# Kernel optimization log

Hardware: AMD Instinct MI355X
Metric: run time of the kernel (lower is better)

## Reference

```python
import jax, jax.numpy as jnp
import numpy as np

N = 100000
E = 1600000
H = 128
M = 256
L = 6
G = 512          # number of graphs in the batch
A = 95           # num_atom_types
EXTRA = 3        # input_dim - 1
EPS = 1e-5


def swish(x):
    return x * jax.nn.sigmoid(x)


def setup_inputs() -> dict:
    key = jax.random.key(0)
    ks = jax.random.split(key, 16)
    z = jax.random.randint(ks[0], (N, 1), 0, A).astype(jnp.float32)
    extra = jax.random.normal(ks[1], (N, EXTRA), dtype=jnp.float32)
    x = jnp.concatenate([z, extra], axis=1)                     # [N, 4]
    edge_index = jax.random.randint(ks[2], (2, E), 0, N)        # [2, E]
    batch = jnp.sort(jax.random.randint(ks[3], (N,), 0, G))     # [N]
    s = 0.02
    z_embed = jax.random.normal(ks[4], (A, H), dtype=jnp.float32) * s
    extra_w = jax.random.normal(ks[5], (H, EXTRA), dtype=jnp.float32) * (1.0 / np.sqrt(EXTRA))
    extra_b = jnp.zeros((H,), jnp.float32)
    conv_w = jax.random.normal(ks[6], (L, H, H), dtype=jnp.float32) * (1.0 / np.sqrt(H))
    conv_b = jnp.zeros((L, H), jnp.float32)
    gamma = jnp.ones((L, H), jnp.float32)
    beta = jnp.zeros((L, H), jnp.float32)
    mean_scale = jnp.ones((L, H), jnp.float32)
    mlp_w1 = jax.random.normal(ks[7], (L, M, H), dtype=jnp.float32) * (1.0 / np.sqrt(H))
    mlp_b1 = jnp.zeros((L, M), jnp.float32)
    mlp_w2 = jax.random.normal(ks[8], (L, H, M), dtype=jnp.float32) * (1.0 / np.sqrt(M))
    mlp_b2 = jnp.zeros((L, H), jnp.float32)
    return dict(x=x, edge_index=edge_index, batch=batch, z_embed=z_embed,
                extra_w=extra_w, extra_b=extra_b, conv_w=conv_w, conv_b=conv_b,
                gamma=gamma, beta=beta, mean_scale=mean_scale,
                mlp_w1=mlp_w1, mlp_b1=mlp_b1, mlp_w2=mlp_w2, mlp_b2=mlp_b2)


def gnn_forward(x, edge_index, batch, z_embed, extra_w, extra_b, conv_w, conv_b,
                gamma, beta, mean_scale, mlp_w1, mlp_b1, mlp_w2, mlp_b2):
    z = x[:, 0].astype(jnp.int32)
    h = z_embed[z] + x[:, 1:] @ extra_w.T + extra_b                 # [N, H]

    # GCN: add self loops, symmetric normalization (computed once; graph is static)
    loop = jnp.arange(N)
    src = jnp.concatenate([edge_index[0], loop])
    dst = jnp.concatenate([edge_index[1], loop])
    deg = jax.ops.segment_sum(jnp.ones_like(dst, jnp.float32), dst, num_segments=N)
    dinv = jnp.where(deg > 0, jax.lax.rsqrt(jnp.maximum(deg, 1.0)), 0.0)
    norm = (dinv[src] * dinv[dst])[:, None]                         # [E+N, 1]

    cnt = jax.ops.segment_sum(jnp.ones((N,), jnp.float32), batch, num_segments=G)[:, None]
    cnt = jnp.maximum(cnt, 1.0)

    for i in range(L):
        h_res = h
        # GCNConv
        xw = h @ conv_w[i].T
        agg = jax.ops.segment_sum(xw[src] * norm, dst, num_segments=N) + conv_b[i]
        # GraphNorm: gamma * (x - alpha*mean) / sqrt(var + eps) + beta, per graph
        mean = jax.ops.segment_sum(agg, batch, num_segments=G) / cnt   # [G, H]
        sub = agg - mean_scale[i] * mean[batch]
        var = jax.ops.segment_sum(sub * sub, batch, num_segments=G) / cnt
        hn = gamma[i] * sub * jax.lax.rsqrt(var[batch] + EPS) + beta[i]
        ha = swish(hn)
        # residual MLP
        h = swish(swish(ha @ mlp_w1[i].T + mlp_b1[i]) @ mlp_w2[i].T + mlp_b2[i]) + h_res
    return h


def reference(x, edge_index, batch, z_embed, extra_w, extra_b, conv_w, conv_b,
              gamma, beta, mean_scale, mlp_w1, mlp_b1, mlp_w2, mlp_b2):
    return gnn_forward(x, edge_index, batch, z_embed, extra_w, extra_b, conv_w, conv_b,
                       gamma, beta, mean_scale, mlp_w1, mlp_b1, mlp_w2, mlp_b2)
```

## Files before the change

kernel.cpp:

```cpp
#include <hip/hip_runtime.h>

#define NN 100000
#define EE 1600000
#define HH 128
#define MM 256
#define LL 6
#define GG 512
#define SCAN_NB ((NN + 1023) / 1024)

typedef __attribute__((ext_vector_type(8))) short short8;
typedef __attribute__((ext_vector_type(4))) float floatx4;

__device__ __forceinline__ float swishf(float v) {
    return v / (1.0f + __expf(-v));
}

__device__ __forceinline__ unsigned short f2bf(float f) {
    unsigned u = __builtin_bit_cast(unsigned, f);
    unsigned r = u + 0x7FFFu + ((u >> 16) & 1u);
    return (unsigned short)(r >> 16);
}

__device__ __forceinline__ float bf2f(unsigned short u) {
    return __builtin_bit_cast(float, (unsigned)u << 16);
}

__device__ __forceinline__ float2 bf2f2(unsigned u) {
    float2 r;
    r.x = __builtin_bit_cast(float, u << 16);
    r.y = __builtin_bit_cast(float, u & 0xFFFF0000u);
    return r;
}

__device__ __forceinline__ void unpack8(uint4 v, float* a) {
    float2 p0 = bf2f2(v.x), p1 = bf2f2(v.y), p2 = bf2f2(v.z), p3 = bf2f2(v.w);
    a[0] = p0.x; a[1] = p0.y; a[2] = p1.x; a[3] = p1.y;
    a[4] = p2.x; a[5] = p2.y; a[6] = p3.x; a[7] = p3.y;
}

__device__ __forceinline__ uint4 pack8(const float* o) {
    uint4 pk;
    pk.x = (unsigned)f2bf(o[0]) | ((unsigned)f2bf(o[1]) << 16);
    pk.y = (unsigned)f2bf(o[2]) | ((unsigned)f2bf(o[3]) << 16);
    pk.z = (unsigned)f2bf(o[4]) | ((unsigned)f2bf(o[5]) << 16);
    pk.w = (unsigned)f2bf(o[6]) | ((unsigned)f2bf(o[7]) << 16);
    return pk;
}

__device__ __forceinline__ uint2 pack4(const float* o) {
    uint2 pk;
    pk.x = (unsigned)f2bf(o[0]) | ((unsigned)f2bf(o[1]) << 16);
    pk.y = (unsigned)f2bf(o[2]) | ((unsigned)f2bf(o[3]) << 16);
    return pk;
}

__global__ void k_embed(const float* __restrict__ x, const float* __restrict__ z_embed,
                        const float* __restrict__ ew, const float* __restrict__ eb,
                        unsigned short* __restrict__ hb) {
    int idx = blockIdx.x * blockDim.x + threadIdx.x;
    if (idx >= NN * 32) return;
    int n = idx >> 5;
    int c0 = (idx & 31) << 2;
    const float* xr = x + (size_t)n * 4;
    int z = (int)xr[0];
    float x1 = xr[1], x2 = xr[2], x3 = xr[3];
    const float* ze = z_embed + (size_t)z * HH + c0;
    float o[4];
#pragma unroll
    for (int j = 0; j < 4; ++j) {
        int c = c0 + j;
        o[j] = ze[j] + x1 * ew[c * 3 + 0] + x2 * ew[c * 3 + 1] + x3 * ew[c * 3 + 2] + eb[c];
    }
    *(uint2*)(hb + (size_t)n * HH + c0) = pack4(o);
}

__global__ void k_f2bf3(const float* __restrict__ s1, unsigned short* __restrict__ d1, int n1,
                        const float* __restrict__ s2, unsigned short* __restrict__ d2, int n2,
                        const float* __restrict__ s3, unsigned short* __restrict__ d3, int n3) {
    int i = blockIdx.x * blockDim.x + threadIdx.x;
    if (i < n1) {
        d1[i] = f2bf(s1[i]);
    } else if (i < n1 + n2) {
        d2[i - n1] = f2bf(s2[i - n1]);
    } else if (i < n1 + n2 + n3) {
        d3[i - n1 - n2] = f2bf(s3[i - n1 - n2]);
    }
}

__global__ __launch_bounds__(256) void k_degree_p(const int* __restrict__ dst,
                                                  int* __restrict__ deg) {
    int part = blockIdx.x & 7;
    int blk = blockIdx.x >> 3;
    int nb = gridDim.x >> 3;
    int lo = (int)((long long)part * NN / 8);
    int hi = (int)((long long)(part + 1) * NN / 8);
    for (int e = blk * 256 + threadIdx.x; e < EE; e += nb * 256) {
        int d = dst[e];
        if (d >= lo && d < hi) atomicAdd(&deg[d], 1);
    }
}

__global__ void k_dinv(const int* __restrict__ deg, float* __restrict__ dinv) {
    int n = blockIdx.x * blockDim.x + threadIdx.x;
    if (n < NN) dinv[n] = rsqrtf((float)(deg[n] + 1));
}

__global__ void k_scan1(const int* __restrict__ deg, int* __restrict__ bsum) {
    __shared__ int sd[256];
    int t = threadIdx.x;
    int base = blockIdx.x * 1024 + t * 4;
    int s = 0;
#pragma unroll
    for (int j = 0; j < 4; ++j) {
        int i = base + j;
        if (i < NN) s += deg[i];
    }
    sd[t] = s;
    __syncthreads();
    for (int off = 128; off > 0; off >>= 1) {
        if (t < off) sd[t] += sd[t + off];
        __syncthreads();
    }
    if (t == 0) bsum[blockIdx.x] = sd[0];
}

__global__ void k_scan2(const int* __restrict__ bsum, int* __restrict__ boff) {
    __shared__ int sd[128];
    int t = threadIdx.x;
    int v = (t < SCAN_NB) ? bsum[t] : 0;
    sd[t] = v;
    __syncthreads();
    for (int off = 1; off < 128; off <<= 1) {
        int u = (t >= off) ? sd[t - off] : 0;
        __syncthreads();
        sd[t] += u;
        __syncthreads();
    }
    boff[t] = sd[t] - v;
}

__global__ void k_scan3(const int* __restrict__ deg, const int* __restrict__ boff,
                        int* __restrict__ rowptr) {
    __shared__ int sd[256];
    int t = threadIdx.x;
    int base = blockIdx.x * 1024 + t * 4;
    int v[4];
    int s = 0;
#pragma unroll
    for (int j = 0; j < 4; ++j) {
        int i = base + j;
        v[j] = (i < NN) ? deg[i] : 0;
        s += v[j];
    }
    sd[t] = s;
    __syncthreads();
    for (int off = 1; off < 256; off <<= 1) {
        int u = (t >= off) ? sd[t - off] : 0;
        __syncthreads();
        sd[t] += u;
        __syncthreads();
    }
    int run = boff[blockIdx.x] + sd[t] - s;
#pragma unroll
    for (int j = 0; j < 4; ++j) {
        int i = base + j;
        if (i < NN) rowptr[i] = run;
        if (i == NN - 1) rowptr[NN] = run + v[j];
        run += v[j];
    }
}

__global__ __launch_bounds__(256) void k_fill_p(const int* __restrict__ ei,
                                                const int* __restrict__ rowptr,
                                                int* __restrict__ cursor,
                                                int* __restrict__ col) {
    int part = blockIdx.x & 7;
    int blk = blockIdx.x >> 3;
    int nb = gridDim.x >> 3;
    int lo = (int)((long long)part * NN / 8);
    int hi = (int)((long long)(part + 1) * NN / 8);
    for (int e = blk * 256 + threadIdx.x; e < EE; e += nb * 256) {
        int d = ei[EE + e];
        if (d >= lo && d < hi) {
            int p = atomicAdd(&cursor[d], 1);
            col[rowptr[d] + p] = ei[e];
        }
    }
}

__global__ void k_gptr(const int* __restrict__ batch, int* __restrict__ gptr) {
    int n = blockIdx.x * blockDim.x + threadIdx.x;
    if (n >= NN) return;
    int b = batch[n];
    int pb = (n == 0) ? -1 : batch[n - 1];
    for (int g = pb + 1; g <= b; ++g) gptr[g] = n;
    if (n == NN - 1) {
        for (int g = b + 1; g <= GG; ++g) gptr[g] = NN;
    }
}

__global__ __launch_bounds__(256) void k_conv(const unsigned short* __restrict__ A,
                                              const unsigned short* __restrict__ B,
                                              const float* __restrict__ dinv,
                                              unsigned short* __restrict__ Cb) {
    __shared__ unsigned short Bs[128][HH + 8];
    const int tid = threadIdx.x;
    const int wave = tid >> 6;
    const int lane = tid & 63;
    const int quad = lane >> 4;
    const int l16 = lane & 15;
    const int wr = (wave & 1) << 6;
    const int wc = (wave >> 1) << 6;
    const int rowBase = blockIdx.x * 128;

    for (int i = tid; i < 128 * (HH / 8); i += 256) {
        int r = i / (HH / 8);
        int kk = (i % (HH / 8)) * 8;
        int rho = (r & 64) | ((r & 3) << 4) | ((r >> 2) & 15);
        *(uint4*)(&Bs[rho][kk]) = *(const uint4*)(B + (size_t)r * HH + kk);
    }

    floatx4 acc[4][4];
    const floatx4 zed = {0.f, 0.f, 0.f, 0.f};
#pragma unroll
    for (int i = 0; i < 4; ++i)
#pragma unroll
        for (int j = 0; j < 4; ++j) acc[i][j] = zed;

    int ar[4];
#pragma unroll
    for (int i = 0; i < 4; ++i) {
        int r = rowBase + wr + (i << 4) + l16;
        ar[i] = r < NN ? r : NN - 1;
    }

    __syncthreads();

#pragma unroll
    for (int ks = 0; ks < HH / 32; ++ks) {
        int k = (ks << 5) + (quad << 3);
        short8 a[4], b[4];
#pragma unroll
        for (int i = 0; i < 4; ++i) a[i] = *(const short8*)(A + (size_t)ar[i] * HH + k);
#pragma unroll
        for (int j = 0; j < 4; ++j) b[j] = *(const short8*)(&Bs[wc + (j << 4) + l16][k]);
#pragma unroll
        for (int i = 0; i < 4; ++i)
#pragma unroll
            for (int j = 0; j < 4; ++j)
                acc[i][j] =
                    __builtin_amdgcn_mfma_f32_16x16x32_bf16(a[i], b[j], acc[i][j], 0, 0, 0);
    }

    const int c0 = wc + (l16 << 2);
#pragma unroll
    for (int i = 0; i < 4; ++i) {
        int rb = rowBase + wr + (i << 4) + (quad << 2);
#pragma unroll
        for (int reg = 0; reg < 4; ++reg) {
            int r = rb + reg;
            if (r < NN) {
                float dv = dinv[r];
                float o[4];
#pragma unroll
                for (int j = 0; j < 4; ++j) o[j] = acc[i][j][reg] * dv;
                *(uint2*)(Cb + (size_t)r * HH + c0) = pack4(o);
            }
        }
    }
}

__global__ __launch_bounds__(256) void k_agg(const unsigned short* __restrict__ y,
                                             const int* __restrict__ rowptr,
                                             const int* __restrict__ col,
                                             const float* __restrict__ dinv,
                                             const float* __restrict__ cb,
                                             unsigned short* __restrict__ agg) {
    int w = threadIdx.x >> 6;
    int lane = threadIdx.x & 63;
    int d = blockIdx.x * 4 + w;
    if (d >= NN) return;
    int grp = lane >> 4;
    int l16 = lane & 15;
    const uint4* yv = (const uint4*)y;
    float acc[8];
#pragma unroll
    for (int j = 0; j < 8; ++j) acc[j] = 0.f;
    if (grp == 0) {
        uint4 v = yv[(size_t)d * 16 + l16];
        unpack8(v, acc);
    }
    int beg = rowptr[d];
    int end = rowptr[d + 1];
    for (int e = beg + grp; e < end; e += 4) {
        int s = col[e];
        uint4 v = yv[(size_t)s * 16 + l16];
        float b0[8];
        unpack8(v, b0);
#pragma unroll
        for (int k = 0; k < 8; ++k) acc[k] += b0[k];
    }
#pragma unroll
    for (int j = 0; j < 8; ++j) {
        acc[j] += __shfl_xor(acc[j], 16, 64);
        acc[j] += __shfl_xor(acc[j], 32, 64);
    }
    if (grp == 0) {
        float dv = dinv[d];
        float4 c0 = *(const float4*)(cb + l16 * 8);
        float4 c1 = *(const float4*)(cb + l16 * 8 + 4);
        float o[8];
        o[0] = acc[0] * dv + c0.x; o[1] = acc[1] * dv + c0.y;
        o[2] = acc[2] * dv + c0.z; o[3] = acc[3] * dv + c0.w;
        o[4] = acc[4] * dv + c1.x; o[5] = acc[5] * dv + c1.y;
        o[6] = acc[6] * dv + c1.z; o[7] = acc[7] * dv + c1.w;
        *(uint4*)(agg + (size_t)d * HH + l16 * 8) = pack8(o);
    }
}

__global__ __launch_bounds__(512) void k_stats(const unsigned short* __restrict__ agg,
                                               const int* __restrict__ gptr,
                                               const float* __restrict__ ms,
                                               const float* __restrict__ gamma,
                                               const float* __restrict__ beta,
                                               float* __restrict__ c1,
                                               float* __restrict__ c0) {
    __shared__ float s1[512];
    __shared__ float s2[512];
    int g = blockIdx.x;
    int t = threadIdx.x;
    int c = t & 127;
    int part = t >> 7;
    int beg = gptr[g];
    int end = gptr[g + 1];
    float S1 = 0.f, S2 = 0.f;
    for (int n = beg + part; n < end; n += 4) {
        float v = bf2f(agg[(size_t)n * HH + c]);
        S1 += v;
        S2 += v * v;
    }
    s1[t] = S1;
    s2[t] = S2;
    __syncthreads();
    if (part == 0) {
        S1 = (s1[c] + s1[c + 128]) + (s1[c + 256] + s1[c + 384]);
        S2 = (s2[c] + s2[c + 128]) + (s2[c + 256] + s2[c + 384]);
        int cnt = end - beg;
        float inv = 1.0f / (float)(cnt > 0 ? cnt : 1);
        float m = S1 * inv;
        float msc = ms[c];
        float var = S2 * inv - msc * (2.0f - msc) * m * m;
        float rstd = rsqrtf(var + 1e-5f);
        float c1v = gamma[c] * rstd;
        c1[g * HH + c] = c1v;
        c0[g * HH + c] = beta[c] - c1v * msc * m;
    }
}

__global__ __launch_bounds__(256) void k_mega(const unsigned short* __restrict__ agg,
                                              const int* __restrict__ batch,
                                              const float* __restrict__ c1,
                                              const float* __restrict__ c0,
                                              const unsigned short* __restrict__ W1,
                                              const float* __restrict__ b1,
                                              const unsigned short* __restrict__ W2,
                                              const float* __restrict__ b2,
                                              const unsigned short* __restrict__ Wc,
                                              const float* __restrict__ dinv,
                                              unsigned short* __restrict__ hb,
                                              float* __restrict__ h_out,
                                              unsigned short* __restrict__ y_out, int writeF,
                                              int doConv) {
    __shared__ unsigned short smem[64 * (MM + 8)];
    const int tid = threadIdx.x;
    const int wave = tid >> 6;
    const int lane = tid & 63;
    const int quad = lane >> 4;
    const int l16 = lane & 15;
    const int wrh = (wave & 1) << 5;
    const int wch = (wave >> 1) << 7;
    const int wc2 = (wave >> 1) << 6;
    const int rowBase = blockIdx.x * 64;
    const floatx4 zed = {0.f, 0.f, 0.f, 0.f};

    int ar[2], gi[2];
#pragma unroll
    for (int i = 0; i < 2; ++i) {
        int r = rowBase + wrh + (i << 4) + l16;
        ar[i] = r < NN ? r : NN - 1;
        gi[i] = batch[ar[i]];
    }

    short8 a_all[4][2];
#pragma unroll
    for (int ks = 0; ks < 4; ++ks) {
        int k = (ks << 5) + (quad << 3);
#pragma unroll
        for (int i = 0; i < 2; ++i) {
            uint4 raw = *(const uint4*)(agg + (size_t)ar[i] * HH + k);
            float v[8];
            unpack8(raw, v);
            const float* c1p = c1 + gi[i] * HH + k;
            const float* c0p = c0 + gi[i] * HH + k;
            float4 c1a = *(const float4*)c1p;
            float4 c1b = *(const float4*)(c1p + 4);
            float4 c0a = *(const float4*)c0p;
            float4 c0b = *(const float4*)(c0p + 4);
            float cc1[8] = {c1a.x, c1a.y, c1a.z, c1a.w, c1b.x, c1b.y, c1b.z, c1b.w};
            float cc0[8] = {c0a.x, c0a.y, c0a.z, c0a.w, c0b.x, c0b.y, c0b.z, c0b.w};
            short8 av;
#pragma unroll
            for (int j = 0; j < 8; ++j)
                av[j] = (short)f2bf(swishf(cc1[j] * v[j] + cc0[j]));
            a_all[ks][i] = av;
        }
    }

    const int c0a = wch + (l16 << 3);
#pragma unroll
    for (int jh = 0; jh < 2; ++jh) {
        floatx4 acc1[2][4];
#pragma unroll
        for (int i = 0; i < 2; ++i)
#pragma unroll
            for (int j = 0; j < 4; ++j) acc1[i][j] = zed;
#pragma unroll
        for (int ks = 0; ks < 4; ++ks) {
            int k = (ks << 5) + (quad << 3);
            short8 b[4];
#pragma unroll
            for (int j = 0; j < 4; ++j) {
                int pc = c0a + (jh << 2) + j;
                b[j] = *(const short8*)(W1 + (size_t)pc * HH + k);
            }
#pragma unroll
            for (int i = 0; i < 2; ++i)
#pragma unroll
                for (int j = 0; j < 4; ++j)
                    acc1[i][j] = __builtin_amdgcn_mfma_f32_16x16x32_bf16(a_all[ks][i], b[j],
                                                                         acc1[i][j], 0, 0, 0);
        }
        float4 b4 = *(const float4*)(b1 + c0a + (jh << 2));
        float bv[4] = {b4.x, b4.y, b4.z, b4.w};
#pragma unroll
        for (int i = 0; i < 2; ++i) {
#pragma unroll
            for (int reg = 0; reg < 4; ++reg) {
                int lr = wrh + (i << 4) + (quad << 2) + reg;
                float o[4];
#pragma unroll
                for (int j = 0; j < 4; ++j) o[j] = swishf(acc1[i][j][reg] + bv[j]);
                *(uint2*)(&smem[lr * (MM + 8) + c0a + (jh << 2)]) = pack4(o);
            }
        }
    }
    __syncthreads();

    floatx4 acc2[2][4];
#pragma unroll
    for (int i = 0; i < 2; ++i)
#pragma unroll
        for (int j = 0; j < 4; ++j) acc2[i][j] = zed;
#pragma unroll
    for (int ks = 0; ks < MM / 32; ++ks) {
        int k = (ks << 5) + (quad << 3);
        short8 a[2], b[4];
#pragma unroll
        for (int i = 0; i < 2; ++i)
            a[i] = *(const short8*)(&smem[(wrh + (i << 4) + l16) * (MM + 8) + k]);
#pragma unroll
        for (int j = 0; j < 4; ++j) {
            int pc = wc2 + (l16 << 2) + j;
            b[j] = *(const short8*)(W2 + (size_t)pc * MM + k);
        }
#pragma unroll
        for (int i = 0; i < 2; ++i)
#pragma unroll
            for (int j = 0; j < 4; ++j)
                acc2[i][j] =
                    __builtin_amdgcn_mfma_f32_16x16x32_bf16(a[i], b[j], acc2[i][j], 0, 0, 0);
    }
    __syncthreads();

    const int co = wc2 + (l16 << 2);
    {
        float4 b4 = *(const float4*)(b2 + co);
        float bv[4] = {b4.x, b4.y, b4.z, b4.w};
#pragma unroll
        for (int i = 0; i < 2; ++i) {
            int rb = rowBase + wrh + (i << 4) + (quad << 2);
#pragma unroll
            for (int reg = 0; reg < 4; ++reg) {
                int r = rb + reg;
                if (r < NN) {
                    uint2 rv = *(const uint2*)(hb + (size_t)r * HH + co);
                    float2 r01 = bf2f2(rv.x), r23 = bf2f2(rv.y);
                    float o[4];
                    o[0] = swishf(acc2[i][0][reg] + bv[0]) + r01.x;
                    o[1] = swishf(acc2[i][1][reg] + bv[1]) + r01.y;
                    o[2] = swishf(acc2[i][2][reg] + bv[2]) + r23.x;
                    o[3] = swishf(acc2[i][3][reg] + bv[3]) + r23.y;
                    uint2 pk = pack4(o);
                    *(uint2*)(hb + (size_t)r * HH + co) = pk;
                    if (writeF)
                        *(float4*)(h_out + (size_t)r * HH + co) =
                            make_float4(o[0], o[1], o[2], o[3]);
                    int lr = wrh + (i << 4) + (quad << 2) + reg;
                    *(uint2*)(&smem[lr * 136 + co]) = pk;
                }
            }
        }
    }

    if (doConv) {
        __syncthreads();
        floatx4 acc3[2][4];
#pragma unroll
        for (int i = 0; i < 2; ++i)
#pragma unroll
            for (int j = 0; j < 4; ++j) acc3[i][j] = zed;
#pragma unroll
        for (int ks = 0; ks < 4; ++ks) {
            int k = (ks << 5) + (quad << 3);
            short8 a[2], b[4];
#pragma unroll
            for (int i = 0; i < 2; ++i)
                a[i] = *(const short8*)(&smem[(wrh + (i << 4) + l16) * 136 + k]);
#pragma unroll
            for (int j = 0; j < 4; ++j) {
                int pc = wc2 + (l16 << 2) + j;
                b[j] = *(const short8*)(Wc + (size_t)pc * HH + k);
            }
#pragma unroll
            for (int i = 0; i < 2; ++i)
#pragma unroll
                for (int j = 0; j < 4; ++j)
                    acc3[i][j] =
                        __builtin_amdgcn_mfma_f32_16x16x32_bf16(a[i], b[j], acc3[i][j], 0, 0, 0);
        }
#pragma unroll
        for (int i = 0; i < 2; ++i) {
            int rb = rowBase + wrh + (i << 4) + (quad << 2);
#pragma unroll
            for (int reg = 0; reg < 4; ++reg) {
                int r = rb + reg;
                if (r < NN) {
                    float dv = dinv[r];
                    float o[4];
#pragma unroll
                    for (int j = 0; j < 4; ++j) o[j] = acc3[i][j][reg] * dv;
                    *(uint2*)(y_out + (size_t)r * HH + co) = pack4(o);
                }
            }
        }
    }
}

extern "C" void kernel_launch(void* const* d_in, const int* in_sizes, int n_in,
                              void* d_out, int out_size, void* d_ws, size_t ws_size,
                              hipStream_t stream) {
    const float* x = (const float*)d_in[0];
    const int* ei = (const int*)d_in[1];
    const int* batch = (const int*)d_in[2];
    const float* z_embed = (const float*)d_in[3];
    const float* extra_w = (const float*)d_in[4];
    const float* extra_b = (const float*)d_in[5];
    const float* conv_w = (const float*)d_in[6];
    const float* conv_b = (const float*)d_in[7];
    const float* gamma = (const float*)d_in[8];
    const float* beta = (const float*)d_in[9];
    const float* mean_scale = (const float*)d_in[10];
    const float* mlp_w1 = (const float*)d_in[11];
    const float* mlp_b1 = (const float*)d_in[12];
    const float* mlp_w2 = (const float*)d_in[13];
    const float* mlp_b2 = (const float*)d_in[14];
    float* h_out = (float*)d_out;

    char* wsB = (char*)d_ws;
    size_t off = 0;
    auto alloc = [&](size_t bytes) -> void* {
        void* p = (void*)(wsB + off);
        off = (off + bytes + 255) & ~(size_t)255;
        return p;
    };
    float* dinv = (float*)alloc((size_t)NN * 4);
    int* deg = (int*)alloc((size_t)NN * 4);
    int* cursor = (int*)alloc((size_t)NN * 4);
    int* rowptr = (int*)alloc((size_t)(NN + 1) * 4);
    int* bsum = (int*)alloc(128 * 4);
    int* boff = (int*)alloc(128 * 4);
    int* col = (int*)alloc((size_t)EE * 4);
    int* gptr = (int*)alloc((size_t)(GG + 1) * 4);
    float* c1t = (float*)alloc((size_t)GG * HH * 4);
    float* c0t = (float*)alloc((size_t)GG * HH * 4);
    unsigned short* wb =
        (unsigned short*)alloc((size_t)(LL * (HH * HH + MM * HH + HH * MM)) * 2);
    unsigned short* cwb = wb;
    unsigned short* w1b = wb + (size_t)LL * HH * HH;
    unsigned short* w2b = w1b + (size_t)LL * MM * HH;
    unsigned short* hb = (unsigned short*)alloc((size_t)NN * HH * 2);
    unsigned short* ybuf = (unsigned short*)alloc((size_t)NN * HH * 2);
    unsigned short* aggb = (unsigned short*)alloc((size_t)NN * HH * 2);

    hipMemsetAsync(deg, 0, (size_t)NN * 4, stream);
    hipMemsetAsync(cursor, 0, (size_t)NN * 4, stream);

    k_embed<<<(NN * 32 + 255) / 256, 256, 0, stream>>>(x, z_embed, extra_w, extra_b, hb);
    {
        int n1 = LL * HH * HH, n2 = LL * MM * HH, n3 = LL * HH * MM;
        int nt = n1 + n2 + n3;
        k_f2bf3<<<(nt + 255) / 256, 256, 0, stream>>>(conv_w, cwb, n1, mlp_w1, w1b, n2,
                                                      mlp_w2, w2b, n3);
    }
    k_degree_p<<<1024, 256, 0, stream>>>(ei + EE, deg);
    k_dinv<<<(NN + 255) / 256, 256, 0, stream>>>(deg, dinv);
    k_scan1<<<SCAN_NB, 256, 0, stream>>>(deg, bsum);
    k_scan2<<<1, 128, 0, stream>>>(bsum, boff);
    k_scan3<<<SCAN_NB, 256, 0, stream>>>(deg, boff, rowptr);
    k_fill_p<<<1024, 256, 0, stream>>>(ei, rowptr, cursor, col);
    k_gptr<<<(NN + 255) / 256, 256, 0, stream>>>(batch, gptr);

    int gconv = (NN + 127) / 128;
    int gmega = (NN + 63) / 64;
    k_conv<<<gconv, 256, 0, stream>>>(hb, cwb, dinv, ybuf);
    for (int i = 0; i < LL; ++i) {
        k_agg<<<(NN + 3) / 4, 256, 0, stream>>>(ybuf, rowptr, col, dinv,
                                                conv_b + (size_t)i * HH, aggb);
        k_stats<<<GG, 512, 0, stream>>>(aggb, gptr, mean_scale + (size_t)i * HH,
                                        gamma + (size_t)i * HH, beta + (size_t)i * HH, c1t,
                                        c0t);
        k_mega<<<gmega, 256, 0, stream>>>(
            aggb, batch, c1t, c0t, w1b + (size_t)i * MM * HH, mlp_b1 + (size_t)i * MM,
            w2b + (size_t)i * HH * MM, mlp_b2 + (size_t)i * HH,
            cwb + (size_t)(i + 1 < LL ? i + 1 : 0) * HH * HH, dinv, hb, h_out, ybuf,
            i == LL - 1 ? 1 : 0, i < LL - 1 ? 1 : 0);
    }
}
```

Baseline: 1.416 ms.

## Stage normalized activations in LDS and retile first MLP GEMM per wave

The GraphNorm+swish prologue is now computed cooperatively (one row-quarter per thread) with coalesced loads and written to a dedicated LDS tile. The first MLP GEMM is retiled so each wave covers all 64 rows by 64 output columns, reading A from LDS. This cuts redundant W1 global loads and the duplicated c1/c0 fetches across waves. The cost is a separate LDS buffer, which raises LDS use and may lower occupancy, plus an extra barrier.

```diff
diff --git a/kernel.cpp b/kernel.cpp
--- a/kernel.cpp
+++ b/kernel.cpp
@@ -371,127 +371,118 @@
                                               float* __restrict__ h_out,
                                               unsigned short* __restrict__ y_out, int writeF,
                                               int doConv) {
-    __shared__ unsigned short smem[64 * (MM + 8)];
+    __shared__ unsigned short ha_s[64 * 136];
+    __shared__ unsigned short ts[64 * 264];
     const int tid = threadIdx.x;
     const int wave = tid >> 6;
     const int lane = tid & 63;
     const int quad = lane >> 4;
     const int l16 = lane & 15;
-    const int wrh = (wave & 1) << 5;
-    const int wch = (wave >> 1) << 7;
-    const int wc2 = (wave >> 1) << 6;
     const int rowBase = blockIdx.x * 64;
     const floatx4 zed = {0.f, 0.f, 0.f, 0.f};
 
-    int ar[2], gi[2];
-#pragma unroll
-    for (int i = 0; i < 2; ++i) {
-        int r = rowBase + wrh + (i << 4) + l16;
-        ar[i] = r < NN ? r : NN - 1;
-        gi[i] = batch[ar[i]];
-    }
-
-    short8 a_all[4][2];
-#pragma unroll
-    for (int ks = 0; ks < 4; ++ks) {
-        int k = (ks << 5) + (quad << 3);
-#pragma unroll
-        for (int i = 0; i < 2; ++i) {
-            uint4 raw = *(const uint4*)(agg + (size_t)ar[i] * HH + k);
+    {
+        int lr = tid >> 2;
+        int coff = (tid & 3) << 5;
+        int r = rowBase + lr;
+        if (r >= NN) r = NN - 1;
+        int g = batch[r];
+        const float* c1p = c1 + g * HH + coff;
+        const float* c0p = c0 + g * HH + coff;
+#pragma unroll
+        for (int q = 0; q < 4; ++q) {
+            uint4 raw = *(const uint4*)(agg + (size_t)r * HH + coff + (q << 3));
             float v[8];
             unpack8(raw, v);
-            const float* c1p = c1 + gi[i] * HH + k;
-            const float* c0p = c0 + gi[i] * HH + k;
-            float4 c1a = *(const float4*)c1p;
-            float4 c1b = *(const float4*)(c1p + 4);
-            float4 c0a = *(const float4*)c0p;
-            float4 c0b = *(const float4*)(c0p + 4);
-            float cc1[8] = {c1a.x, c1a.y, c1a.z, c1a.w, c1b.x, c1b.y, c1b.z, c1b.w};
-            float cc0[8] = {c0a.x, c0a.y, c0a.z, c0a.w, c0b.x, c0b.y, c0b.z, c0b.w};
-            short8 av;
-#pragma unroll
-            for (int j = 0; j < 8; ++j)
-                av[j] = (short)f2bf(swishf(cc1[j] * v[j] + cc0[j]));
-            a_all[ks][i] = av;
-        }
-    }
-
-    const int c0a = wch + (l16 << 3);
-#pragma unroll
-    for (int jh = 0; jh < 2; ++jh) {
-        floatx4 acc1[2][4];
-#pragma unroll
-        for (int i = 0; i < 2; ++i)
+            float4 ca = *(const float4*)(c1p + (q << 3));
+            float4 cb4 = *(const float4*)(c1p + (q << 3) + 4);
+            float4 da = *(const float4*)(c0p + (q << 3));
+            float4 db = *(const float4*)(c0p + (q << 3) + 4);
+            float cc1[8] = {ca.x, ca.y, ca.z, ca.w, cb4.x, cb4.y, cb4.z, cb4.w};
+            float cc0[8] = {da.x, da.y, da.z, da.w, db.x, db.y, db.z, db.w};
+            float o[8];
+#pragma unroll
+            for (int j = 0; j < 8; ++j) o[j] = swishf(cc1[j] * v[j] + cc0[j]);
+            *(uint4*)(&ha_s[lr * 136 + coff + (q << 3)]) = pack8(o);
+        }
+    }
+    __syncthreads();
+
+    {
+        const int wca = wave << 6;
+        floatx4 acc1[4][4];
+#pragma unroll
+        for (int i = 0; i < 4; ++i)
 #pragma unroll
             for (int j = 0; j < 4; ++j) acc1[i][j] = zed;
 #pragma unroll
         for (int ks = 0; ks < 4; ++ks) {
             int k = (ks << 5) + (quad << 3);
-            short8 b[4];
-#pragma unroll
-            for (int j = 0; j < 4; ++j) {
-                int pc = c0a + (jh << 2) + j;
-                b[j] = *(const short8*)(W1 + (size_t)pc * HH + k);
+            short8 a[4], b[4];
+#pragma unroll
+            for (int i = 0; i < 4; ++i)
+                a[i] = *(const short8*)(&ha_s[((i << 4) + l16) * 136 + k]);
+#pragma unroll
+            for (int j = 0; j < 4; ++j)
+                b[j] = *(const short8*)(W1 + (size_t)(wca + (l16 << 2) + j) * HH + k);
+#pragma unroll
+            for (int i = 0; i < 4; ++i)
+#pragma unroll
+                for (int j = 0; j < 4; ++j)
+                    acc1[i][j] =
+                        __builtin_amdgcn_mfma_f32_16x16x32_bf16(a[i], b[j], acc1[i][j], 0, 0, 0);
+        }
+        const int ct = wca + (l16 << 2);
+        float4 b4 = *(const float4*)(b1 + ct);
+        float bv[4] = {b4.x, b4.y, b4.z, b4.w};
+#pragma unroll
+        for (int i = 0; i < 4; ++i) {
+#pragma unroll
+            for (int reg = 0; reg < 4; ++reg) {
+                int lr = (i << 4) + (quad << 2) + reg;
+                float o[4];
+#pragma unroll
+                for (int j = 0; j < 4; ++j) o[j] = swishf(acc1[i][j][reg] + bv[j]);
+                *(uint2*)(&ts[lr * 264 + ct]) = pack4(o);
             }
+        }
+    }
+    __syncthreads();
+
+    const int wrb = (wave & 1) << 5;
+    const int wcb = (wave >> 1) << 6;
+    const int co = wcb + (l16 << 2);
+    {
+        floatx4 acc2[2][4];
+#pragma unroll
+        for (int i = 0; i < 2; ++i)
+#pragma unroll
+            for (int j = 0; j < 4; ++j) acc2[i][j] = zed;
+#pragma unroll
+        for (int ks = 0; ks < 8; ++ks) {
+            int k = (ks << 5) + (quad << 3);
+            short8 a[2], b[4];
 #pragma unroll
             for (int i = 0; i < 2; ++i)
+                a[i] = *(const short8*)(&ts[(wrb + (i << 4) + l16) * 264 + k]);
+#pragma unroll
+            for (int j = 0; j < 4; ++j)
+                b[j] = *(const short8*)(W2 + (size_t)(wcb + (l16 << 2) + j) * MM + k);
+#pragma unroll
+            for (int i = 0; i < 2; ++i)
 #pragma unroll
                 for (int j = 0; j < 4; ++j)
-                    acc1[i][j] = __builtin_amdgcn_mfma_f32_16x16x32_bf16(a_all[ks][i], b[j],
-                                                                         acc1[i][j], 0, 0, 0);
-        }
-        float4 b4 = *(const float4*)(b1 + c0a + (jh << 2));
-        float bv[4] = {b4.x, b4.y, b4.z, b4.w};
-#pragma unroll
-        for (int i = 0; i < 2; ++i) {
-#pragma unroll
-            for (int reg = 0; reg < 4; ++reg) {
-                int lr = wrh + (i << 4) + (quad << 2) + reg;
-                float o[4];
-#pragma unroll
-                for (int j = 0; j < 4; ++j) o[j] = swishf(acc1[i][j][reg] + bv[j]);
-                *(uint2*)(&smem[lr * (MM + 8) + c0a + (jh << 2)]) = pack4(o);
-            }
-        }
-    }
-    __syncthreads();
-
-    floatx4 acc2[2][4];
-#pragma unroll
-    for (int i = 0; i < 2; ++i)
-#pragma unroll
-        for (int j = 0; j < 4; ++j) acc2[i][j] = zed;
-#pragma unroll
-    for (int ks = 0; ks < MM / 32; ++ks) {
-        int k = (ks << 5) + (quad << 3);
-        short8 a[2], b[4];
-#pragma unroll
-        for (int i = 0; i < 2; ++i)
-            a[i] = *(const short8*)(&smem[(wrh + (i << 4) + l16) * (MM + 8) + k]);
-#pragma unroll
-        for (int j = 0; j < 4; ++j) {
-            int pc = wc2 + (l16 << 2) + j;
-            b[j] = *(const short8*)(W2 + (size_t)pc * MM + k);
-        }
-#pragma unroll
-        for (int i = 0; i < 2; ++i)
-#pragma unroll
-            for (int j = 0; j < 4; ++j)
-                acc2[i][j] =
-                    __builtin_amdgcn_mfma_f32_16x16x32_bf16(a[i], b[j], acc2[i][j], 0, 0, 0);
-    }
-    __syncthreads();
-
-    const int co = wc2 + (l16 << 2);
-    {
+                    acc2[i][j] =
+                        __builtin_amdgcn_mfma_f32_16x16x32_bf16(a[i], b[j], acc2[i][j], 0, 0, 0);
+        }
         float4 b4 = *(const float4*)(b2 + co);
         float bv[4] = {b4.x, b4.y, b4.z, b4.w};
 #pragma unroll
         for (int i = 0; i < 2; ++i) {
-            int rb = rowBase + wrh + (i << 4) + (quad << 2);
 #pragma unroll
             for (int reg = 0; reg < 4; ++reg) {
-                int r = rb + reg;
+                int lr = wrb + (i << 4) + (quad << 2) + reg;
+                int r = rowBase + lr;
                 if (r < NN) {
                     uint2 rv = *(const uint2*)(hb + (size_t)r * HH + co);
                     float2 r01 = bf2f2(rv.x), r23 = bf2f2(rv.y);
@@ -505,8 +496,9 @@
                     if (writeF)
                         *(float4*)(h_out + (size_t)r * HH + co) =
                             make_float4(o[0], o[1], o[2], o[3]);
-                    int lr = wrh + (i << 4) + (quad << 2) + reg;
-                    *(uint2*)(&smem[lr * 136 + co]) = pk;
+                    *(uint2*)(&ha_s[lr * 136 + co]) = pk;
+                } else {
+                    *(uint2*)(&ha_s[lr * 136 + co]) = make_uint2(0u, 0u);
                 }
             }
         }
@@ -525,12 +517,10 @@
             short8 a[2], b[4];
 #pragma unroll
             for (int i = 0; i < 2; ++i)
-                a[i] = *(const short8*)(&smem[(wrh + (i << 4) + l16) * 136 + k]);
-#pragma unroll
-            for (int j = 0; j < 4; ++j) {
-                int pc = wc2 + (l16 << 2) + j;
-                b[j] = *(const short8*)(Wc + (size_t)pc * HH + k);
-            }
+                a[i] = *(const short8*)(&ha_s[(wrb + (i << 4) + l16) * 136 + k]);
+#pragma unroll
+            for (int j = 0; j < 4; ++j)
+                b[j] = *(const short8*)(Wc + (size_t)(wcb + (l16 << 2) + j) * HH + k);
 #pragma unroll
             for (int i = 0; i < 2; ++i)
 #pragma unroll
@@ -540,10 +530,9 @@
         }
 #pragma unroll
         for (int i = 0; i < 2; ++i) {
-            int rb = rowBase + wrh + (i << 4) + (quad << 2);
 #pragma unroll
             for (int reg = 0; reg < 4; ++reg) {
-                int r = rb + reg;
+                int r = rowBase + wrb + (i << 4) + (quad << 2) + reg;
                 if (r < NN) {
                     float dv = dinv[r];
                     float o[4];
```

Result: faster. 1.346 ms (-4.9%).
